# Performance work log

Measured on AMD Instinct MI355X. Metric: run time of the kernel, lower is better.

## Reference

```python
import jax, jax.numpy as jnp
import numpy as np
import math

B, L, D = 2, 4096, 1024
H, DK, DV = 4, 256, 256
CS = 32          # delta-rule chunk size
CONV = 4         # short conv kernel
FIR_S, FIR_L = 3, 31
GIN = D + 3 * DV # 1792 gate input dim
GH = D * 2 // 2  # 1024 gate hidden dim
MIN_LOCAL = 0.05


def dwconv(x, w):
    """Causal depthwise conv. x: [b,l,C], w: [C,k] -> [b,l,C]."""
    k = w.shape[-1]
    xf = jnp.pad(jnp.swapaxes(x, 1, 2), ((0, 0), (0, 0), (k - 1, 0)))
    y = jax.lax.conv_general_dilated(xf, w[:, None, :], (1,), 'VALID',
                                     dimension_numbers=('NCH', 'OIH', 'NCH'),
                                     feature_group_count=w.shape[0])
    return jnp.swapaxes(y, 1, 2)


def l2n(x):
    return x * jax.lax.rsqrt(jnp.sum(x * x, -1, keepdims=True) + 1e-12)


def delta_rule(q, k, v, beta):
    """Chunkwise O(N) delta rule. q,k: [b,h,L,dk], v: [b,h,L,dv], beta: [b,h,L]."""
    b, h, Lq, dk = q.shape
    dv = v.shape[-1]
    n = Lq // CS
    q, k = l2n(q), l2n(k)
    v = v * beta[..., None]
    kb = k * beta[..., None]
    rs = lambda t: t.reshape(b, h, n, CS, t.shape[-1])
    q, k, v, kb = rs(q), rs(k), rs(v), rs(kb)
    # block-local inverse of unit-lower-triangular (I + strict_lower(kb k^T))
    strict_lo = jnp.tril(jnp.ones((CS, CS), bool), -1)
    A = jnp.where(strict_lo, kb @ jnp.swapaxes(k, -1, -2), 0.0)
    eye = jnp.eye(CS, dtype=q.dtype)
    Tinv = jax.scipy.linalg.solve_triangular(
        eye + A, jnp.broadcast_to(eye, A.shape), lower=True, unit_diagonal=True)
    u = Tinv @ v
    w = Tinv @ kb
    strict_up = jnp.triu(jnp.ones((CS, CS), bool), 1)

    def step(S, xs):
        q_i, k_i, u_i, w_i = xs
        attn = jnp.where(strict_up, 0.0, q_i @ jnp.swapaxes(k_i, -1, -2))
        u_i = u_i - w_i @ S
        o_i = q_i @ S + attn @ u_i
        S = S + jnp.swapaxes(k_i, -1, -2) @ u_i
        return S, o_i

    mv = lambda t: jnp.moveaxis(t, 2, 0)  # scan over chunks
    S0 = jnp.zeros((b, h, dk, dv), q.dtype)
    _, out = jax.lax.scan(step, S0, (mv(q), mv(k), mv(u), mv(w)))
    return jnp.moveaxis(out, 0, 2).reshape(b, h, Lq, dv)


def _forward(hidden_states, q_proj_w, k_proj_w, v_proj_w, b_proj_w,
             q_conv_w, k_conv_w, v_conv_w, fir_short_w, fir_long_w,
             fg_w1, fg_b1, fg_w2, fg_b2, logit_temp, o_norm_w, o_proj_w):
    b, l, _ = hidden_states.shape
    hs = hidden_states
    q = jax.nn.silu(dwconv(hs @ q_proj_w.T, q_conv_w)).reshape(b, l, H, DK)
    k = jax.nn.silu(dwconv(hs @ k_proj_w.T, k_conv_w)).reshape(b, l, H, DK)
    v = jax.nn.silu(dwconv(hs @ v_proj_w.T, v_conv_w)).reshape(b, l, H, DV)
    beta = jax.nn.sigmoid(hs @ b_proj_w.T)  # [b,l,h]
    tr = lambda t: jnp.swapaxes(t, 1, 2)
    delta = tr(delta_rule(tr(q), tr(k), tr(v), jnp.swapaxes(beta, 1, 2)))
    fir = lambda x, w: dwconv(x.reshape(b, l, H * DV),
                              w.reshape(H * DV, -1)).reshape(b, l, H, DV)
    short = fir(v, fir_short_w)
    long_ = fir(v, fir_long_w)
    gate_in = jnp.concatenate([hs, short.mean(2), long_.mean(2), delta.mean(2)], -1)
    logits = jax.nn.gelu(gate_in @ fg_w1.T + fg_b1, approximate=False) @ fg_w2.T + fg_b2
    temp = jax.nn.softplus(logit_temp) + 1e-4
    wgt = jax.nn.softmax(logits / temp, -1)[:, :, None, :]  # [b,l,1,4]
    wgt = jnp.broadcast_to(wgt, (b, l, H, 4))
    # floor on local-path weights proportional to direct-value weight, renormalize
    floor = MIN_LOCAL * wgt[..., 3:4]
    wloc = jnp.maximum(wgt[..., :2], floor)
    wgt = jnp.concatenate([wloc, wgt[..., 2:]], -1)
    wgt = wgt / wgt.sum(-1, keepdims=True)
    o = (wgt[..., 0:1] * short + wgt[..., 1:2] * long_ +
         wgt[..., 2:3] * delta + wgt[..., 3:4] * v)
    # RMSNorm over head_v_dim
    o = o * jax.lax.rsqrt(jnp.mean(o * o, -1, keepdims=True) + 1e-5) * o_norm_w
    return o.reshape(b, l, H * DV) @ o_proj_w.T


def setup_inputs() -> dict:
    key = jax.random.key(0)
    ks = jax.random.split(key, 12)
    s = 0.02
    return {
        'hidden_states': jax.random.normal(ks[0], (B, L, D), jnp.float32),
        'q_proj_w': jax.random.normal(ks[1], (H * DK, D), jnp.float32) * s,
        'k_proj_w': jax.random.normal(ks[2], (H * DK, D), jnp.float32) * s,
        'v_proj_w': jax.random.normal(ks[3], (H * DV, D), jnp.float32) * s,
        'b_proj_w': jax.random.normal(ks[4], (H, D), jnp.float32) * s,
        'q_conv_w': jax.random.normal(ks[5], (H * DK, CONV), jnp.float32) * s,
        'k_conv_w': jax.random.normal(ks[6], (H * DK, CONV), jnp.float32) * s,
        'v_conv_w': jax.random.normal(ks[7], (H * DV, CONV), jnp.float32) * s,
        'fir_short_w': jnp.zeros((H, DV, FIR_S), jnp.float32).at[..., -1].set(1.0),
        'fir_long_w': jnp.zeros((H, DV, FIR_L), jnp.float32).at[..., -1].set(1.0),
        'fg_w1': jax.random.normal(ks[8], (GH, GIN), jnp.float32) * s,
        'fg_b1': jnp.zeros((GH,), jnp.float32),
        'fg_w2': jax.random.normal(ks[9], (4, GH), jnp.float32) * s,
        'fg_b2': jnp.array([-0.2, -0.2, 1.0, 3.0], jnp.float32),
        'logit_temp': jnp.full((1,), math.log(math.expm1(0.7)), jnp.float32),
        'o_norm_w': jnp.ones((DV,), jnp.float32),
        'o_proj_w': jax.random.normal(ks[10], (D, H * DV), jnp.float32) * s,
    }


def reference(hidden_states, q_proj_w, k_proj_w, v_proj_w, b_proj_w,
              q_conv_w, k_conv_w, v_conv_w, fir_short_w, fir_long_w,
              fg_w1, fg_b1, fg_w2, fg_b2, logit_temp, o_norm_w, o_proj_w):
    return _forward(hidden_states, q_proj_w, k_proj_w, v_proj_w, b_proj_w,
                    q_conv_w, k_conv_w, v_conv_w, fir_short_w, fir_long_w,
                    fg_w1, fg_b1, fg_w2, fg_b2, logit_temp, o_norm_w, o_proj_w)
```

## Files before the change

### kernel.cpp

```cpp
#include <hip/hip_runtime.h>
#include <cstdint>
#include <cstddef>

namespace {
constexpr int LB   = 4096;
constexpr int CS   = 32;
constexpr int NCH  = 128;
constexpr int GINC = 1792;
constexpr int GHC  = 1024;
}

__device__ __forceinline__ float dot4(float4 a, float4 b) {
  return a.x*b.x + a.y*b.y + a.z*b.z + a.w*b.w;
}

__global__ __launch_bounds__(256)
void gemm_bt(const float* __restrict__ A, const float* __restrict__ W,
             float* __restrict__ C, int M, int N, int K) {
  __shared__ float As[16][128];
  __shared__ float Bs[16][128];
  const int tid = threadIdx.x;
  const int bn = blockIdx.x * 128;
  const int bm = blockIdx.y * 128;
  const int tx = tid & 15, ty = tid >> 4;
  const int lr = tid >> 1, lk = (tid & 1) * 8;

  float acc[8][8];
  #pragma unroll
  for (int i = 0; i < 8; ++i)
    #pragma unroll
    for (int j = 0; j < 8; ++j) acc[i][j] = 0.f;

  const float* Ap = A + (size_t)(bm + lr) * K + lk;
  const float* Wp = W + (size_t)(bn + lr) * K + lk;

  for (int k0 = 0; k0 < K; k0 += 16) {
    float4 a0 = *(const float4*)(Ap + k0);
    float4 a1 = *(const float4*)(Ap + k0 + 4);
    float4 b0 = *(const float4*)(Wp + k0);
    float4 b1 = *(const float4*)(Wp + k0 + 4);
    __syncthreads();
    As[lk+0][lr]=a0.x; As[lk+1][lr]=a0.y; As[lk+2][lr]=a0.z; As[lk+3][lr]=a0.w;
    As[lk+4][lr]=a1.x; As[lk+5][lr]=a1.y; As[lk+6][lr]=a1.z; As[lk+7][lr]=a1.w;
    Bs[lk+0][lr]=b0.x; Bs[lk+1][lr]=b0.y; Bs[lk+2][lr]=b0.z; Bs[lk+3][lr]=b0.w;
    Bs[lk+4][lr]=b1.x; Bs[lk+5][lr]=b1.y; Bs[lk+6][lr]=b1.z; Bs[lk+7][lr]=b1.w;
    __syncthreads();
    #pragma unroll
    for (int kk = 0; kk < 16; ++kk) {
      float av[8], bv[8];
      *(float4*)(av)   = *(const float4*)&As[kk][ty*8];
      *(float4*)(av+4) = *(const float4*)&As[kk][ty*8+4];
      *(float4*)(bv)   = *(const float4*)&Bs[kk][tx*8];
      *(float4*)(bv+4) = *(const float4*)&Bs[kk][tx*8+4];
      #pragma unroll
      for (int i = 0; i < 8; ++i)
        #pragma unroll
        for (int j = 0; j < 8; ++j) acc[i][j] += av[i]*bv[j];
    }
  }

  #pragma unroll
  for (int i = 0; i < 8; ++i) {
    float* cp = C + (size_t)(bm + ty*8 + i) * N + bn + tx*8;
    *(float4*)cp     = make_float4(acc[i][0],acc[i][1],acc[i][2],acc[i][3]);
    *(float4*)(cp+4) = make_float4(acc[i][4],acc[i][5],acc[i][6],acc[i][7]);
  }
}

__global__ __launch_bounds__(256)
void gemm_gate(const float* __restrict__ hs, const float* __restrict__ sh,
               const float* __restrict__ lo, const float* __restrict__ de,
               const float* __restrict__ W, const float* __restrict__ bias,
               float* __restrict__ C) {
  const int M = LB, N = GHC, K = GINC;
  __shared__ float As[16][128];
  __shared__ float Bs[16][128];
  const int tid = threadIdx.x;
  const int bn = blockIdx.x * 128;
  const int bm = blockIdx.y * 128;
  const int tx = tid & 15, ty = tid >> 4;
  const int lr = tid >> 1, lk = (tid & 1) * 8;

  float acc[8][8];
  #pragma unroll
  for (int i = 0; i < 8; ++i)
    #pragma unroll
    for (int j = 0; j < 8; ++j) acc[i][j] = 0.f;

  const size_t arow = (size_t)(bm + lr) * 1024;
  const float* Wp = W + (size_t)(bn + lr) * K + lk;

  for (int k0 = 0; k0 < K; k0 += 16) {
    const int col = k0 + lk;
    float4 a0, a1;
    if (col < 1024) {
      const float* p = hs + arow + col;
      a0 = *(const float4*)p; a1 = *(const float4*)(p + 4);
    } else {
      const int sec = (col - 1024) >> 8;
      const int d   = (col - 1024) & 255;
      const float* p = (sec == 0 ? sh : (sec == 1 ? lo : de)) + arow + d;
      float4 q0 = *(const float4*)(p);       float4 q1 = *(const float4*)(p+4);
      float4 r0 = *(const float4*)(p+256);   float4 r1 = *(const float4*)(p+260);
      float4 s0 = *(const float4*)(p+512);   float4 s1 = *(const float4*)(p+516);
      float4 t0 = *(const float4*)(p+768);   float4 t1 = *(const float4*)(p+772);
      a0 = make_float4(0.25f*(q0.x+r0.x+s0.x+t0.x), 0.25f*(q0.y+r0.y+s0.y+t0.y),
                       0.25f*(q0.z+r0.z+s0.z+t0.z), 0.25f*(q0.w+r0.w+s0.w+t0.w));
      a1 = make_float4(0.25f*(q1.x+r1.x+s1.x+t1.x), 0.25f*(q1.y+r1.y+s1.y+t1.y),
                       0.25f*(q1.z+r1.z+s1.z+t1.z), 0.25f*(q1.w+r1.w+s1.w+t1.w));
    }
    float4 b0 = *(const float4*)(Wp + k0);
    float4 b1 = *(const float4*)(Wp + k0 + 4);
    __syncthreads();
    As[lk+0][lr]=a0.x; As[lk+1][lr]=a0.y; As[lk+2][lr]=a0.z; As[lk+3][lr]=a0.w;
    As[lk+4][lr]=a1.x; As[lk+5][lr]=a1.y; As[lk+6][lr]=a1.z; As[lk+7][lr]=a1.w;
    Bs[lk+0][lr]=b0.x; Bs[lk+1][lr]=b0.y; Bs[lk+2][lr]=b0.z; Bs[lk+3][lr]=b0.w;
    Bs[lk+4][lr]=b1.x; Bs[lk+5][lr]=b1.y; Bs[lk+6][lr]=b1.z; Bs[lk+7][lr]=b1.w;
    __syncthreads();
    #pragma unroll
    for (int kk = 0; kk < 16; ++kk) {
      float av[8], bv[8];
      *(float4*)(av)   = *(const float4*)&As[kk][ty*8];
      *(float4*)(av+4) = *(const float4*)&As[kk][ty*8+4];
      *(float4*)(bv)   = *(const float4*)&Bs[kk][tx*8];
      *(float4*)(bv+4) = *(const float4*)&Bs[kk][tx*8+4];
      #pragma unroll
      for (int i = 0; i < 8; ++i)
        #pragma unroll
        for (int j = 0; j < 8; ++j) acc[i][j] += av[i]*bv[j];
    }
  }

  float bvals[8];
  #pragma unroll
  for (int j = 0; j < 8; ++j) bvals[j] = bias[bn + tx*8 + j];
  #pragma unroll
  for (int i = 0; i < 8; ++i) {
    float* cp = C + (size_t)(bm + ty*8 + i) * N + bn + tx*8;
    float out[8];
    #pragma unroll
    for (int j = 0; j < 8; ++j) {
      float v = acc[i][j] + bvals[j];
      out[j] = 0.5f * v * (1.0f + erff(v * 0.70710678118654752f));
    }
    *(float4*)cp     = make_float4(out[0],out[1],out[2],out[3]);
    *(float4*)(cp+4) = make_float4(out[4],out[5],out[6],out[7]);
  }
}

__global__ __launch_bounds__(256)
void conv_silu_k(const float* __restrict__ x, const float* __restrict__ w,
                 float* __restrict__ y) {
  int idx = blockIdx.x * 256 + threadIdx.x;
  int c = idx & 1023;
  int l = idx >> 10;
  float w0 = w[c*4+0], w1 = w[c*4+1], w2 = w[c*4+2], w3 = w[c*4+3];
  float acc = x[(size_t)l*1024 + c] * w3;
  if (l >= 1) acc += x[(size_t)(l-1)*1024 + c] * w2;
  if (l >= 2) acc += x[(size_t)(l-2)*1024 + c] * w1;
  if (l >= 3) acc += x[(size_t)(l-3)*1024 + c] * w0;
  y[idx] = acc / (1.f + expf(-acc));
}

__global__ __launch_bounds__(256)
void beta_k(const float* __restrict__ hs, const float* __restrict__ bw,
            float* __restrict__ beta) {
  int row = blockIdx.x * 4 + (threadIdx.x >> 6);
  int ln  = threadIdx.x & 63;
  const float* xp = hs + (size_t)row * 1024 + ln*16;
  float a[4] = {0.f,0.f,0.f,0.f};
  #pragma unroll
  for (int t = 0; t < 4; ++t) {
    float4 xv = *(const float4*)(xp + t*4);
    #pragma unroll
    for (int h = 0; h < 4; ++h) {
      float4 wv = *(const float4*)(bw + (size_t)h*1024 + ln*16 + t*4);
      a[h] += dot4(xv, wv);
    }
  }
  #pragma unroll
  for (int h = 0; h < 4; ++h) {
    #pragma unroll
    for (int off = 32; off > 0; off >>= 1) a[h] += __shfl_xor(a[h], off, 64);
  }
  if (ln == 0) {
    #pragma unroll
    for (int h = 0; h < 4; ++h)
      beta[(size_t)row*4 + h] = 1.f / (1.f + expf(-a[h]));
  }
}

__global__ __launch_bounds__(256)
void delta_pre(float* __restrict__ q, float* __restrict__ k,
               const float* __restrict__ v, const float* __restrict__ beta,
               float* __restrict__ u, float* __restrict__ w,
               float* __restrict__ attn) {
  __shared__ float qs[32][260];
  __shared__ float ks[32][260];
  __shared__ float vs[32][260];
  __shared__ float Am[32][33];
  __shared__ float Ti[32][33];
  __shared__ float red[32][8];
  __shared__ float bet[32];

  const int bid = blockIdx.x;
  const int h  = bid & 3;
  const int c  = bid >> 2;
  const int tid = threadIdx.x;
  const int r  = tid >> 3;
  const int sg = tid & 7;

  const size_t base = (size_t)(c * CS) * 1024 + h * 256;
  float* qrow = q + base + (size_t)r * 1024 + sg * 32;
  float* krow = k + base + (size_t)r * 1024 + sg * 32;
  const float* vrow = v + base + (size_t)r * 1024 + sg * 32;

  #pragma unroll
  for (int t = 0; t < 8; ++t) {
    *(float4*)&qs[r][sg*32 + t*4] = *(const float4*)(qrow + t*4);
    *(float4*)&ks[r][sg*32 + t*4] = *(const float4*)(krow + t*4);
    *(float4*)&vs[r][sg*32 + t*4] = *(const float4*)(vrow + t*4);
  }
  if (tid < 32) bet[tid] = beta[(size_t)(c * CS + tid) * 4 + h];
  __syncthreads();

  {
    float p = 0.f;
    #pragma unroll
    for (int i = 0; i < 32; ++i) { float x = qs[r][sg*32+i]; p += x*x; }
    red[r][sg] = p;
  }
  __syncthreads();
  {
    float s = 1e-12f;
    #pragma unroll
    for (int i = 0; i < 8; ++i) s += red[r][i];
    float qn = rsqrtf(s);
    #pragma unroll
    for (int t = 0; t < 8; ++t) {
      float4 vq = *(float4*)&qs[r][sg*32 + t*4];
      vq.x*=qn; vq.y*=qn; vq.z*=qn; vq.w*=qn;
      *(float4*)&qs[r][sg*32 + t*4] = vq;
      *(float4*)(qrow + t*4) = vq;
    }
    float bb = bet[r];
    #pragma unroll
    for (int t = 0; t < 8; ++t) {
      float4 vv = *(float4*)&vs[r][sg*32 + t*4];
      vv.x*=bb; vv.y*=bb; vv.z*=bb; vv.w*=bb;
      *(float4*)&vs[r][sg*32 + t*4] = vv;
    }
  }
  __syncthreads();
  {
    float p = 0.f;
    #pragma unroll
    for (int i = 0; i < 32; ++i) { float x = ks[r][sg*32+i]; p += x*x; }
    red[r][sg] = p;
  }
  __syncthreads();
  {
    float s = 1e-12f;
    #pragma unroll
    for (int i = 0; i < 8; ++i) s += red[r][i];
    float kn = rsqrtf(s);
    #pragma unroll
    for (int t = 0; t < 8; ++t) {
      float4 vq = *(float4*)&ks[r][sg*32 + t*4];
      vq.x*=kn; vq.y*=kn; vq.z*=kn; vq.w*=kn;
      *(float4*)&ks[r][sg*32 + t*4] = vq;
      *(float4*)(krow + t*4) = vq;
    }
  }
  __syncthreads();

  {
    const int ti = tid >> 4, tj = tid & 15;
    const int r0 = ti*2, s0 = tj*2;
    float kk00=0,kk01=0,kk10=0,kk11=0,qk00=0,qk01=0,qk10=0,qk11=0;
    for (int d4 = 0; d4 < 64; ++d4) {
      float4 kr0 = *(const float4*)&ks[r0  ][d4*4];
      float4 kr1 = *(const float4*)&ks[r0+1][d4*4];
      float4 qr0 = *(const float4*)&qs[r0  ][d4*4];
      float4 qr1 = *(const float4*)&qs[r0+1][d4*4];
      float4 kc0 = *(const float4*)&ks[s0  ][d4*4];
      float4 kc1 = *(const float4*)&ks[s0+1][d4*4];
      kk00 += dot4(kr0,kc0); kk01 += dot4(kr0,kc1);
      kk10 += dot4(kr1,kc0); kk11 += dot4(kr1,kc1);
      qk00 += dot4(qr0,kc0); qk01 += dot4(qr0,kc1);
      qk10 += dot4(qr1,kc0); qk11 += dot4(qr1,kc1);
    }
    Am[r0  ][s0  ] = (r0   > s0  ) ? bet[r0  ]*kk00 : 0.f;
    Am[r0  ][s0+1] = (r0   > s0+1) ? bet[r0  ]*kk01 : 0.f;
    Am[r0+1][s0  ] = (r0+1 > s0  ) ? bet[r0+1]*kk10 : 0.f;
    Am[r0+1][s0+1] = (r0+1 > s0+1) ? bet[r0+1]*kk11 : 0.f;
    float* ap = attn + ((size_t)(h * NCH + c)) * 1024;
    ap[(r0  )*32 + s0  ] = (r0   >= s0  ) ? qk00 : 0.f;
    ap[(r0  )*32 + s0+1] = (r0   >= s0+1) ? qk01 : 0.f;
    ap[(r0+1)*32 + s0  ] = (r0+1 >= s0  ) ? qk10 : 0.f;
    ap[(r0+1)*32 + s0+1] = (r0+1 >= s0+1) ? qk11 : 0.f;
  }
  __syncthreads();

  if (tid < 32) {
    const int cc = tid;
    Ti[cc][cc] = 1.f;
    for (int rr = cc+1; rr < 32; ++rr) {
      float s = Am[rr][cc];
      for (int ss = cc+1; ss < rr; ++ss) s += Am[rr][ss] * Ti[ss][cc];
      Ti[rr][cc] = -s;
    }
  }
  __syncthreads();

  {
    float out[32];
    #pragma unroll
    for (int i = 0; i < 32; ++i) out[i] = vs[r][sg*32+i];
    for (int s2 = 0; s2 < r; ++s2) {
      float t = Ti[r][s2];
      #pragma unroll
      for (int t4 = 0; t4 < 8; ++t4) {
        float4 vv = *(const float4*)&vs[s2][sg*32 + t4*4];
        out[t4*4+0] += t*vv.x; out[t4*4+1] += t*vv.y;
        out[t4*4+2] += t*vv.z; out[t4*4+3] += t*vv.w;
      }
    }
    float* up = u + base + (size_t)r*1024 + sg*32;
    #pragma unroll
    for (int t4 = 0; t4 < 8; ++t4)
      *(float4*)(up + t4*4) = make_float4(out[t4*4],out[t4*4+1],out[t4*4+2],out[t4*4+3]);
  }
  {
    float out[32];
    float br = bet[r];
    #pragma unroll
    for (int i = 0; i < 32; ++i) out[i] = br * ks[r][sg*32+i];
    for (int s2 = 0; s2 < r; ++s2) {
      float t = Ti[r][s2] * bet[s2];
      #pragma unroll
      for (int t4 = 0; t4 < 8; ++t4) {
        float4 vv = *(const float4*)&ks[s2][sg*32 + t4*4];
        out[t4*4+0] += t*vv.x; out[t4*4+1] += t*vv.y;
        out[t4*4+2] += t*vv.z; out[t4*4+3] += t*vv.w;
      }
    }
    float* wp = w + base + (size_t)r*1024 + sg*32;
    #pragma unroll
    for (int t4 = 0; t4 < 8; ++t4)
      *(float4*)(wp + t4*4) = make_float4(out[t4*4],out[t4*4+1],out[t4*4+2],out[t4*4+3]);
  }
}

__device__ __forceinline__ void smul8(const float* __restrict__ row,
                                      const float* __restrict__ Sb,
                                      float acc[8]) {
  #pragma unroll
  for (int i4 = 0; i4 < 8; ++i4) {
    float4 wq = *(const float4*)(row + i4*4);
    float wv[4] = {wq.x, wq.y, wq.z, wq.w};
    #pragma unroll
    for (int t = 0; t < 4; ++t) {
      const float* sp = Sb + (i4*4 + t)*8;
      float4 s0 = *(const float4*)sp;
      float4 s1 = *(const float4*)(sp + 4);
      acc[0] += wv[t]*s0.x; acc[1] += wv[t]*s0.y;
      acc[2] += wv[t]*s0.z; acc[3] += wv[t]*s0.w;
      acc[4] += wv[t]*s1.x; acc[5] += wv[t]*s1.y;
      acc[6] += wv[t]*s1.z; acc[7] += wv[t]*s1.w;
    }
  }
}

__global__ __launch_bounds__(256)
void delta_scan(const float* __restrict__ q, const float* __restrict__ k,
                const float* __restrict__ w, const float* __restrict__ u,
                const float* __restrict__ attn, float* __restrict__ o) {
  __shared__ float ws_[32][260];
  __shared__ float qs[32][260];
  __shared__ float ks[32][260];
  __shared__ float Ssh[8*260];
  __shared__ float red[32][8][8];
  __shared__ float un[32][8];
  __shared__ float us[32][8];
  __shared__ float at[32][36];

  const int bid = blockIdx.x;
  const int h  = bid & 3;
  const int g  = bid >> 2;
  const int tid = threadIdx.x;
  const int r  = tid >> 3;
  const int sg = tid & 7;

  const size_t base = (size_t)h * 256;

  for (int i = tid; i < 8*260; i += 256) Ssh[i] = 0.f;

  for (int c = 0; c < NCH; ++c) {
    const size_t rowbase = base + (size_t)(c * CS) * 1024;
    const float* qp = q + rowbase + (size_t)r*1024 + sg*32;
    const float* kp = k + rowbase + (size_t)r*1024 + sg*32;
    const float* wp = w + rowbase + (size_t)r*1024 + sg*32;
    float4 qreg[8], kreg[8], wreg[8];
    #pragma unroll
    for (int t = 0; t < 8; ++t) {
      qreg[t] = *(const float4*)(qp + t*4);
      kreg[t] = *(const float4*)(kp + t*4);
      wreg[t] = *(const float4*)(wp + t*4);
    }
    float uval = u[rowbase + (size_t)r*1024 + g*8 + sg];
    float4 areg = *(const float4*)(attn + ((size_t)(h*NCH + c))*1024 + tid*4);

    __syncthreads();
    #pragma unroll
    for (int t = 0; t < 8; ++t) {
      *(float4*)&qs[r][sg*32 + t*4] = qreg[t];
      *(float4*)&ks[r][sg*32 + t*4] = kreg[t];
      *(float4*)&ws_[r][sg*32 + t*4] = wreg[t];
    }
    us[r][sg] = uval;
    at[r][sg*4+0] = areg.x; at[r][sg*4+1] = areg.y;
    at[r][sg*4+2] = areg.z; at[r][sg*4+3] = areg.w;
    __syncthreads();

    {
      float acc[8];
      #pragma unroll
      for (int j = 0; j < 8; ++j) acc[j] = 0.f;
      smul8(&ws_[r][sg*32], &Ssh[sg*260], acc);
      *(float4*)&red[r][sg][0] = make_float4(acc[0],acc[1],acc[2],acc[3]);
      *(float4*)&red[r][sg][4] = make_float4(acc[4],acc[5],acc[6],acc[7]);
    }
    __syncthreads();
    {
      float t = 0.f;
      #pragma unroll
      for (int o2 = 0; o2 < 8; ++o2) t += red[r][o2][sg];
      un[r][sg] = us[r][sg] - t;
    }
    __syncthreads();
    {
      float acc[8];
      #pragma unroll
      for (int j = 0; j < 8; ++j) acc[j] = 0.f;
      smul8(&qs[r][sg*32], &Ssh[sg*260], acc);
      #pragma unroll
      for (int t2 = 0; t2 < 4; ++t2) {
        int s2 = sg*4 + t2;
        float a = at[r][s2];
        float4 u0 = *(const float4*)&un[s2][0];
        float4 u1 = *(const float4*)&un[s2][4];
        acc[0] += a*u0.x; acc[1] += a*u0.y; acc[2] += a*u0.z; acc[3] += a*u0.w;
        acc[4] += a*u1.x; acc[5] += a*u1.y; acc[6] += a*u1.z; acc[7] += a*u1.w;
      }
      *(float4*)&red[r][sg][0] = make_float4(acc[0],acc[1],acc[2],acc[3]);
      *(float4*)&red[r][sg][4] = make_float4(acc[4],acc[5],acc[6],acc[7]);
    }
    __syncthreads();
    {
      float t = 0.f;
      #pragma unroll
      for (int o2 = 0; o2 < 8; ++o2) t += red[r][o2][sg];
      o[rowbase + (size_t)r*1024 + g*8 + sg] = t;
    }
    {
      const int dk = tid;
      float a2[8];
      #pragma unroll
      for (int j = 0; j < 8; ++j) a2[j] = 0.f;
      #pragma unroll 4
      for (int r2 = 0; r2 < 32; ++r2) {
        float kv = ks[r2][dk];
        float4 u0 = *(const float4*)&un[r2][0];
        float4 u1 = *(const float4*)&un[r2][4];
        a2[0] += kv*u0.x; a2[1] += kv*u0.y; a2[2] += kv*u0.z; a2[3] += kv*u0.w;
        a2[4] += kv*u1.x; a2[5] += kv*u1.y; a2[6] += kv*u1.z; a2[7] += kv*u1.w;
      }
      float* sp = &Ssh[(dk>>5)*260 + (dk&31)*8];
      float4 s0 = *(float4*)sp, s1 = *(float4*)(sp+4);
      s0.x += a2[0]; s0.y += a2[1]; s0.z += a2[2]; s0.w += a2[3];
      s1.x += a2[4]; s1.y += a2[5]; s1.z += a2[6]; s1.w += a2[7];
      *(float4*)sp = s0; *(float4*)(sp+4) = s1;
    }
  }
}

template<int KF>
__global__ __launch_bounds__(256)
void fir_k(const float* __restrict__ x, const float* __restrict__ wf,
           float* __restrict__ y) {
  int idx = blockIdx.x * 256 + threadIdx.x;
  int c = idx & 1023;
  int l = idx >> 10;
  const float* wp = wf + (size_t)c * KF;
  float acc = 0.f;
  #pragma unroll
  for (int j = 0; j < KF; ++j) {
    int ls = l - (KF-1) + j;
    if (ls >= 0) acc += x[(size_t)ls*1024 + c] * wp[j];
  }
  y[idx] = acc;
}

__global__ __launch_bounds__(256)
void logit_k(const float* __restrict__ hid, const float* __restrict__ w2,
             const float* __restrict__ b2, const float* __restrict__ lt,
             float* __restrict__ wgt) {
  int row = blockIdx.x * 4 + (threadIdx.x >> 6);
  int ln  = threadIdx.x & 63;
  const float* hp = hid + (size_t)row * 1024 + ln*16;
  float a[4] = {0.f,0.f,0.f,0.f};
  #pragma unroll
  for (int t = 0; t < 4; ++t) {
    float4 hv = *(const float4*)(hp + t*4);
    #pragma unroll
    for (int cc = 0; cc < 4; ++cc) {
      float4 wv = *(const float4*)(w2 + (size_t)cc*1024 + ln*16 + t*4);
      a[cc] += dot4(hv, wv);
    }
  }
  #pragma unroll
  for (int cc = 0; cc < 4; ++cc) {
    #pragma unroll
    for (int off = 32; off > 0; off >>= 1) a[cc] += __shfl_xor(a[cc], off, 64);
  }
  if (ln == 0) {
    float x = lt[0];
    float temp = (x > 20.f ? x : log1pf(expf(x))) + 1e-4f;
    float lg[4];
    #pragma unroll
    for (int cc = 0; cc < 4; ++cc) lg[cc] = (a[cc] + b2[cc]) / temp;
    float m = fmaxf(fmaxf(lg[0],lg[1]), fmaxf(lg[2],lg[3]));
    float e0 = expf(lg[0]-m), e1 = expf(lg[1]-m), e2 = expf(lg[2]-m), e3 = expf(lg[3]-m);
    float inv = 1.f / (e0+e1+e2+e3);
    float s0 = e0*inv, s1 = e1*inv, s2 = e2*inv, s3 = e3*inv;
    float fl = 0.05f * s3;
    float w0 = fmaxf(s0, fl), w1 = fmaxf(s1, fl);
    float tot = 1.f / (w0 + w1 + s2 + s3);
    float* wp = wgt + (size_t)row*4;
    wp[0] = w0*tot; wp[1] = w1*tot; wp[2] = s2*tot; wp[3] = s3*tot;
  }
}

__global__ __launch_bounds__(256)
void mix_k(const float* __restrict__ sh, const float* __restrict__ lo,
           const float* __restrict__ de, const float* __restrict__ v,
           const float* __restrict__ wgt, const float* __restrict__ onw,
           float* __restrict__ o) {
  int bid = blockIdx.x;
  int l = bid >> 2, h = bid & 3;
  int d = threadIdx.x;
  size_t off = (size_t)l*1024 + h*256 + d;
  const float* wp = wgt + (size_t)l*4;
  float w0 = wp[0], w1 = wp[1], w2 = wp[2], w3 = wp[3];
  float val = w0*sh[off] + w1*lo[off] + w2*de[off] + w3*v[off];
  __shared__ float rd[4];
  float ss = val*val;
  #pragma unroll
  for (int m = 32; m > 0; m >>= 1) ss += __shfl_xor(ss, m, 64);
  if ((threadIdx.x & 63) == 0) rd[threadIdx.x >> 6] = ss;
  __syncthreads();
  float tot = rd[0] + rd[1] + rd[2] + rd[3];
  float sc = rsqrtf(tot * (1.f/256.f) + 1e-5f);
  o[off] = val * sc * onw[d];
}

extern "C" void kernel_launch(void* const* d_in, const int* in_sizes, int n_in,
                              void* d_out, int out_size, void* d_ws, size_t ws_size,
                              hipStream_t stream) {
  (void)in_sizes; (void)n_in; (void)out_size; (void)ws_size;
  const float* hs   = (const float*)d_in[0];
  const float* qw   = (const float*)d_in[1];
  const float* kw   = (const float*)d_in[2];
  const float* vw   = (const float*)d_in[3];
  const float* bw   = (const float*)d_in[4];
  const float* qcw  = (const float*)d_in[5];
  const float* kcw  = (const float*)d_in[6];
  const float* vcw  = (const float*)d_in[7];
  const float* fsw  = (const float*)d_in[8];
  const float* flw  = (const float*)d_in[9];
  const float* fgw1 = (const float*)d_in[10];
  const float* fgb1 = (const float*)d_in[11];
  const float* fgw2 = (const float*)d_in[12];
  const float* fgb2 = (const float*)d_in[13];
  const float* ltmp = (const float*)d_in[14];
  const float* onw  = (const float*)d_in[15];
  const float* ow   = (const float*)d_in[16];

  float* ws0 = (float*)d_ws;
  const size_t SZB = (size_t)LB * 1024;
  float* A    = ws0;
  float* qb   = ws0 + SZB;
  float* kb2  = ws0 + 2*SZB;
  float* vb   = ws0 + 3*SZB;
  float* ub   = ws0 + 4*SZB;
  float* wb   = ws0 + 5*SZB;
  float* att  = ws0 + 6*SZB;
  float* betab= att + (size_t)4*NCH*1024;
  float* wgtb = betab + (size_t)LB*4;

  dim3 blk(256);
  dim3 gg(1024/128, LB/128);
  const int ELT = LB*1024/256;

  for (int b = 0; b < 2; ++b) {
    const float* hsb = hs + (size_t)b * LB * 1024;
    float* outb = (float*)d_out + (size_t)b * LB * 1024;

    gemm_bt<<<gg, blk, 0, stream>>>(hsb, qw, A, LB, 1024, 1024);
    conv_silu_k<<<dim3(ELT), blk, 0, stream>>>(A, qcw, qb);
    gemm_bt<<<gg, blk, 0, stream>>>(hsb, kw, A, LB, 1024, 1024);
    conv_silu_k<<<dim3(ELT), blk, 0, stream>>>(A, kcw, kb2);
    gemm_bt<<<gg, blk, 0, stream>>>(hsb, vw, A, LB, 1024, 1024);
    conv_silu_k<<<dim3(ELT), blk, 0, stream>>>(A, vcw, vb);

    beta_k<<<dim3(LB/4), blk, 0, stream>>>(hsb, bw, betab);
    delta_pre<<<dim3(512), blk, 0, stream>>>(qb, kb2, vb, betab, ub, wb, att);
    delta_scan<<<dim3(128), blk, 0, stream>>>(qb, kb2, wb, ub, att, A);

    fir_k<3><<<dim3(ELT), blk, 0, stream>>>(vb, fsw, qb);
    fir_k<31><<<dim3(ELT), blk, 0, stream>>>(vb, flw, kb2);

    gemm_gate<<<gg, blk, 0, stream>>>(hsb, qb, kb2, A, fgw1, fgb1, ub);
    logit_k<<<dim3(LB/4), blk, 0, stream>>>(ub, fgw2, fgb2, ltmp, wgtb);
    mix_k<<<dim3(LB*4), blk, 0, stream>>>(qb, kb2, A, vb, wgtb, onw, wb);

    gemm_bt<<<gg, blk, 0, stream>>>(wb, ow, outb, LB, 1024, 1024);
  }
}
```

Baseline: 5.468 ms.

## Batch delta-rule kernels across both sequences and shorten the scan critical path

When the workspace is large enough, q/k/v/u/w buffers for both batch elements are kept so delta_pre and delta_scan run once over the batch with twice as many blocks. This fills more of the GPU during the serial scan. delta_pre now precomputes q - attn·w per chunk, so each scan step needs one fused pass over the state and one reduction instead of two dependent rounds with extra barriers. It also rotates the shared-memory access order to reduce bank conflicts. The cost is a larger workspace requirement and a fallback path that keeps the old per-batch schedule.

```diff
diff --git a/kernel.cpp b/kernel.cpp
--- a/kernel.cpp
+++ b/kernel.cpp
@@ -8,6 +8,7 @@
 constexpr int NCH  = 128;
 constexpr int GINC = 1792;
 constexpr int GHC  = 1024;
+constexpr size_t SZB = (size_t)LB * 1024;
 }
 
 __device__ __forceinline__ float dot4(float4 a, float4 b) {
@@ -72,7 +73,7 @@
                const float* __restrict__ lo, const float* __restrict__ de,
                const float* __restrict__ W, const float* __restrict__ bias,
                float* __restrict__ C) {
-  const int M = LB, N = GHC, K = GINC;
+  const int N = GHC, K = GINC;
   __shared__ float As[16][128];
   __shared__ float Bs[16][128];
   const int tid = threadIdx.x;
@@ -200,28 +201,31 @@
   __shared__ float vs[32][260];
   __shared__ float Am[32][33];
   __shared__ float Ti[32][33];
+  __shared__ float ats[32][33];
   __shared__ float red[32][8];
   __shared__ float bet[32];
 
   const int bid = blockIdx.x;
+  const int b  = bid >> 9;
   const int h  = bid & 3;
-  const int c  = bid >> 2;
+  const int c  = (bid >> 2) & 127;
   const int tid = threadIdx.x;
   const int r  = tid >> 3;
   const int sg = tid & 7;
 
-  const size_t base = (size_t)(c * CS) * 1024 + h * 256;
+  const size_t base = (size_t)b * SZB + (size_t)(c * CS) * 1024 + h * 256;
   float* qrow = q + base + (size_t)r * 1024 + sg * 32;
   float* krow = k + base + (size_t)r * 1024 + sg * 32;
   const float* vrow = v + base + (size_t)r * 1024 + sg * 32;
 
   #pragma unroll
   for (int t = 0; t < 8; ++t) {
-    *(float4*)&qs[r][sg*32 + t*4] = *(const float4*)(qrow + t*4);
-    *(float4*)&ks[r][sg*32 + t*4] = *(const float4*)(krow + t*4);
-    *(float4*)&vs[r][sg*32 + t*4] = *(const float4*)(vrow + t*4);
-  }
-  if (tid < 32) bet[tid] = beta[(size_t)(c * CS + tid) * 4 + h];
+    int tr = (t + sg) & 7;
+    *(float4*)&qs[r][sg*32 + tr*4] = *(const float4*)(qrow + tr*4);
+    *(float4*)&ks[r][sg*32 + tr*4] = *(const float4*)(krow + tr*4);
+    *(float4*)&vs[r][sg*32 + tr*4] = *(const float4*)(vrow + tr*4);
+  }
+  if (tid < 32) bet[tid] = beta[((size_t)b*LB + c*CS + tid)*4 + h];
   __syncthreads();
 
   {
@@ -238,17 +242,18 @@
     float qn = rsqrtf(s);
     #pragma unroll
     for (int t = 0; t < 8; ++t) {
-      float4 vq = *(float4*)&qs[r][sg*32 + t*4];
+      int tr = (t + sg) & 7;
+      float4 vq = *(float4*)&qs[r][sg*32 + tr*4];
       vq.x*=qn; vq.y*=qn; vq.z*=qn; vq.w*=qn;
-      *(float4*)&qs[r][sg*32 + t*4] = vq;
-      *(float4*)(qrow + t*4) = vq;
+      *(float4*)&qs[r][sg*32 + tr*4] = vq;
     }
     float bb = bet[r];
     #pragma unroll
     for (int t = 0; t < 8; ++t) {
-      float4 vv = *(float4*)&vs[r][sg*32 + t*4];
+      int tr = (t + sg) & 7;
+      float4 vv = *(float4*)&vs[r][sg*32 + tr*4];
       vv.x*=bb; vv.y*=bb; vv.z*=bb; vv.w*=bb;
-      *(float4*)&vs[r][sg*32 + t*4] = vv;
+      *(float4*)&vs[r][sg*32 + tr*4] = vv;
     }
   }
   __syncthreads();
@@ -266,10 +271,11 @@
     float kn = rsqrtf(s);
     #pragma unroll
     for (int t = 0; t < 8; ++t) {
-      float4 vq = *(float4*)&ks[r][sg*32 + t*4];
+      int tr = (t + sg) & 7;
+      float4 vq = *(float4*)&ks[r][sg*32 + tr*4];
       vq.x*=kn; vq.y*=kn; vq.z*=kn; vq.w*=kn;
-      *(float4*)&ks[r][sg*32 + t*4] = vq;
-      *(float4*)(krow + t*4) = vq;
+      *(float4*)&ks[r][sg*32 + tr*4] = vq;
+      *(float4*)(krow + tr*4) = vq;
     }
   }
   __syncthreads();
@@ -294,11 +300,17 @@
     Am[r0  ][s0+1] = (r0   > s0+1) ? bet[r0  ]*kk01 : 0.f;
     Am[r0+1][s0  ] = (r0+1 > s0  ) ? bet[r0+1]*kk10 : 0.f;
     Am[r0+1][s0+1] = (r0+1 > s0+1) ? bet[r0+1]*kk11 : 0.f;
-    float* ap = attn + ((size_t)(h * NCH + c)) * 1024;
-    ap[(r0  )*32 + s0  ] = (r0   >= s0  ) ? qk00 : 0.f;
-    ap[(r0  )*32 + s0+1] = (r0   >= s0+1) ? qk01 : 0.f;
-    ap[(r0+1)*32 + s0  ] = (r0+1 >= s0  ) ? qk10 : 0.f;
-    ap[(r0+1)*32 + s0+1] = (r0+1 >= s0+1) ? qk11 : 0.f;
+    float a00 = (r0   >= s0  ) ? qk00 : 0.f;
+    float a01 = (r0   >= s0+1) ? qk01 : 0.f;
+    float a10 = (r0+1 >= s0  ) ? qk10 : 0.f;
+    float a11 = (r0+1 >= s0+1) ? qk11 : 0.f;
+    ats[r0  ][s0  ] = a00;  ats[r0  ][s0+1] = a01;
+    ats[r0+1][s0  ] = a10;  ats[r0+1][s0+1] = a11;
+    float* ap = attn + (((size_t)b*4 + h) * NCH + c) * 1024;
+    ap[(r0  )*32 + s0  ] = a00;
+    ap[(r0  )*32 + s0+1] = a01;
+    ap[(r0+1)*32 + s0  ] = a10;
+    ap[(r0+1)*32 + s0+1] = a11;
   }
   __syncthreads();
 
@@ -316,14 +328,18 @@
   {
     float out[32];
     #pragma unroll
-    for (int i = 0; i < 32; ++i) out[i] = vs[r][sg*32+i];
+    for (int t = 0; t < 8; ++t) {
+      int tr = (t + sg) & 7;
+      *(float4*)&out[tr*4] = *(const float4*)&vs[r][sg*32 + tr*4];
+    }
     for (int s2 = 0; s2 < r; ++s2) {
       float t = Ti[r][s2];
       #pragma unroll
       for (int t4 = 0; t4 < 8; ++t4) {
-        float4 vv = *(const float4*)&vs[s2][sg*32 + t4*4];
-        out[t4*4+0] += t*vv.x; out[t4*4+1] += t*vv.y;
-        out[t4*4+2] += t*vv.z; out[t4*4+3] += t*vv.w;
+        int tr = (t4 + sg) & 7;
+        float4 vv = *(const float4*)&vs[s2][sg*32 + tr*4];
+        out[tr*4+0] += t*vv.x; out[tr*4+1] += t*vv.y;
+        out[tr*4+2] += t*vv.z; out[tr*4+3] += t*vv.w;
       }
     }
     float* up = u + base + (size_t)r*1024 + sg*32;
@@ -331,6 +347,8 @@
     for (int t4 = 0; t4 < 8; ++t4)
       *(float4*)(up + t4*4) = make_float4(out[t4*4],out[t4*4+1],out[t4*4+2],out[t4*4+3]);
   }
+  __syncthreads();
+
   {
     float out[32];
     float br = bet[r];
@@ -340,35 +358,41 @@
       float t = Ti[r][s2] * bet[s2];
       #pragma unroll
       for (int t4 = 0; t4 < 8; ++t4) {
-        float4 vv = *(const float4*)&ks[s2][sg*32 + t4*4];
-        out[t4*4+0] += t*vv.x; out[t4*4+1] += t*vv.y;
-        out[t4*4+2] += t*vv.z; out[t4*4+3] += t*vv.w;
+        int tr = (t4 + sg) & 7;
+        float4 vv = *(const float4*)&ks[s2][sg*32 + tr*4];
+        out[tr*4+0] += t*vv.x; out[tr*4+1] += t*vv.y;
+        out[tr*4+2] += t*vv.z; out[tr*4+3] += t*vv.w;
       }
     }
     float* wp = w + base + (size_t)r*1024 + sg*32;
     #pragma unroll
+    for (int t4 = 0; t4 < 8; ++t4) {
+      *(float4*)(wp + t4*4) = make_float4(out[t4*4],out[t4*4+1],out[t4*4+2],out[t4*4+3]);
+      *(float4*)&vs[r][sg*32 + t4*4] = *(const float4*)&out[t4*4];
+    }
+  }
+  __syncthreads();
+
+  {
+    float out[32];
+    #pragma unroll
+    for (int t = 0; t < 8; ++t) {
+      int tr = (t + sg) & 7;
+      *(float4*)&out[tr*4] = *(const float4*)&qs[r][sg*32 + tr*4];
+    }
+    for (int s2 = 0; s2 <= r; ++s2) {
+      float a = ats[r][s2];
+      #pragma unroll
+      for (int t4 = 0; t4 < 8; ++t4) {
+        int tr = (t4 + sg) & 7;
+        float4 vv = *(const float4*)&vs[s2][sg*32 + tr*4];
+        out[tr*4+0] -= a*vv.x; out[tr*4+1] -= a*vv.y;
+        out[tr*4+2] -= a*vv.z; out[tr*4+3] -= a*vv.w;
+      }
+    }
+    #pragma unroll
     for (int t4 = 0; t4 < 8; ++t4)
-      *(float4*)(wp + t4*4) = make_float4(out[t4*4],out[t4*4+1],out[t4*4+2],out[t4*4+3]);
-  }
-}
-
-__device__ __forceinline__ void smul8(const float* __restrict__ row,
-                                      const float* __restrict__ Sb,
-                                      float acc[8]) {
-  #pragma unroll
-  for (int i4 = 0; i4 < 8; ++i4) {
-    float4 wq = *(const float4*)(row + i4*4);
-    float wv[4] = {wq.x, wq.y, wq.z, wq.w};
-    #pragma unroll
-    for (int t = 0; t < 4; ++t) {
-      const float* sp = Sb + (i4*4 + t)*8;
-      float4 s0 = *(const float4*)sp;
-      float4 s1 = *(const float4*)(sp + 4);
-      acc[0] += wv[t]*s0.x; acc[1] += wv[t]*s0.y;
-      acc[2] += wv[t]*s0.z; acc[3] += wv[t]*s0.w;
-      acc[4] += wv[t]*s1.x; acc[5] += wv[t]*s1.y;
-      acc[6] += wv[t]*s1.z; acc[7] += wv[t]*s1.w;
-    }
+      *(float4*)(qrow + t4*4) = make_float4(out[t4*4],out[t4*4+1],out[t4*4+2],out[t4*4+3]);
   }
 }
 
@@ -380,19 +404,21 @@
   __shared__ float qs[32][260];
   __shared__ float ks[32][260];
   __shared__ float Ssh[8*260];
-  __shared__ float red[32][8][8];
+  __shared__ float red[2][32][68];
   __shared__ float un[32][8];
-  __shared__ float us[32][8];
+  __shared__ float us[32][12];
   __shared__ float at[32][36];
 
   const int bid = blockIdx.x;
+  const int b  = bid >> 7;
   const int h  = bid & 3;
-  const int g  = bid >> 2;
+  const int g  = (bid >> 2) & 31;
   const int tid = threadIdx.x;
   const int r  = tid >> 3;
   const int sg = tid & 7;
 
-  const size_t base = (size_t)h * 256;
+  const size_t base = (size_t)b * SZB + (size_t)h * 256;
+  const size_t aoff = ((size_t)b*4 + h) * NCH * 1024;
 
   for (int i = tid; i < 8*260; i += 256) Ssh[i] = 0.f;
 
@@ -409,14 +435,15 @@
       wreg[t] = *(const float4*)(wp + t*4);
     }
     float uval = u[rowbase + (size_t)r*1024 + g*8 + sg];
-    float4 areg = *(const float4*)(attn + ((size_t)(h*NCH + c))*1024 + tid*4);
+    float4 areg = *(const float4*)(attn + aoff + (size_t)c*1024 + tid*4);
 
     __syncthreads();
     #pragma unroll
     for (int t = 0; t < 8; ++t) {
-      *(float4*)&qs[r][sg*32 + t*4] = qreg[t];
-      *(float4*)&ks[r][sg*32 + t*4] = kreg[t];
-      *(float4*)&ws_[r][sg*32 + t*4] = wreg[t];
+      int tr = (t + sg) & 7;
+      *(float4*)&qs[r][sg*32 + tr*4]  = qreg[tr];
+      *(float4*)&ks[r][sg*32 + tr*4]  = kreg[tr];
+      *(float4*)&ws_[r][sg*32 + tr*4] = wreg[tr];
     }
     us[r][sg] = uval;
     at[r][sg*4+0] = areg.x; at[r][sg*4+1] = areg.y;
@@ -424,45 +451,59 @@
     __syncthreads();
 
     {
-      float acc[8];
-      #pragma unroll
-      for (int j = 0; j < 8; ++j) acc[j] = 0.f;
-      smul8(&ws_[r][sg*32], &Ssh[sg*260], acc);
-      *(float4*)&red[r][sg][0] = make_float4(acc[0],acc[1],acc[2],acc[3]);
-      *(float4*)&red[r][sg][4] = make_float4(acc[4],acc[5],acc[6],acc[7]);
+      float accw[8], accq[8];
+      #pragma unroll
+      for (int j = 0; j < 8; ++j) { accw[j] = 0.f; accq[j] = 0.f; }
+      #pragma unroll
+      for (int t2 = 0; t2 < 4; ++t2) {
+        int s2 = sg*4 + ((t2 + r) & 3);
+        float a = at[r][s2];
+        float4 u0 = *(const float4*)&us[s2][0];
+        float4 u1 = *(const float4*)&us[s2][4];
+        accq[0] += a*u0.x; accq[1] += a*u0.y; accq[2] += a*u0.z; accq[3] += a*u0.w;
+        accq[4] += a*u1.x; accq[5] += a*u1.y; accq[6] += a*u1.z; accq[7] += a*u1.w;
+      }
+      #pragma unroll
+      for (int i4 = 0; i4 < 8; ++i4) {
+        int ir = (i4 + sg) & 7;
+        float4 wq = *(const float4*)&ws_[r][sg*32 + ir*4];
+        float4 qq = *(const float4*)&qs[r][sg*32 + ir*4];
+        float wv[4] = {wq.x,wq.y,wq.z,wq.w};
+        float qv[4] = {qq.x,qq.y,qq.z,qq.w};
+        #pragma unroll
+        for (int t = 0; t < 4; ++t) {
+          const float* sp = &Ssh[sg*260 + (ir*4 + t)*8];
+          float4 s0 = *(const float4*)sp;
+          float4 s1 = *(const float4*)(sp + 4);
+          accw[0] += wv[t]*s0.x; accw[1] += wv[t]*s0.y;
+          accw[2] += wv[t]*s0.z; accw[3] += wv[t]*s0.w;
+          accw[4] += wv[t]*s1.x; accw[5] += wv[t]*s1.y;
+          accw[6] += wv[t]*s1.z; accw[7] += wv[t]*s1.w;
+          accq[0] += qv[t]*s0.x; accq[1] += qv[t]*s0.y;
+          accq[2] += qv[t]*s0.z; accq[3] += qv[t]*s0.w;
+          accq[4] += qv[t]*s1.x; accq[5] += qv[t]*s1.y;
+          accq[6] += qv[t]*s1.z; accq[7] += qv[t]*s1.w;
+        }
+      }
+      *(float4*)&red[0][r][sg*8]     = make_float4(accw[0],accw[1],accw[2],accw[3]);
+      *(float4*)&red[0][r][sg*8+4]   = make_float4(accw[4],accw[5],accw[6],accw[7]);
+      *(float4*)&red[1][r][sg*8]     = make_float4(accq[0],accq[1],accq[2],accq[3]);
+      *(float4*)&red[1][r][sg*8+4]   = make_float4(accq[4],accq[5],accq[6],accq[7]);
     }
     __syncthreads();
+
     {
-      float t = 0.f;
-      #pragma unroll
-      for (int o2 = 0; o2 < 8; ++o2) t += red[r][o2][sg];
-      un[r][sg] = us[r][sg] - t;
+      float tw = 0.f, tq = 0.f;
+      #pragma unroll
+      for (int o2 = 0; o2 < 8; ++o2) {
+        tw += red[0][r][o2*8 + sg];
+        tq += red[1][r][o2*8 + sg];
+      }
+      un[r][sg] = us[r][sg] - tw;
+      o[rowbase + (size_t)r*1024 + g*8 + sg] = tq;
     }
     __syncthreads();
-    {
-      float acc[8];
-      #pragma unroll
-      for (int j = 0; j < 8; ++j) acc[j] = 0.f;
-      smul8(&qs[r][sg*32], &Ssh[sg*260], acc);
-      #pragma unroll
-      for (int t2 = 0; t2 < 4; ++t2) {
-        int s2 = sg*4 + t2;
-        float a = at[r][s2];
-        float4 u0 = *(const float4*)&un[s2][0];
-        float4 u1 = *(const float4*)&un[s2][4];
-        acc[0] += a*u0.x; acc[1] += a*u0.y; acc[2] += a*u0.z; acc[3] += a*u0.w;
-        acc[4] += a*u1.x; acc[5] += a*u1.y; acc[6] += a*u1.z; acc[7] += a*u1.w;
-      }
-      *(float4*)&red[r][sg][0] = make_float4(acc[0],acc[1],acc[2],acc[3]);
-      *(float4*)&red[r][sg][4] = make_float4(acc[4],acc[5],acc[6],acc[7]);
-    }
-    __syncthreads();
-    {
-      float t = 0.f;
-      #pragma unroll
-      for (int o2 = 0; o2 < 8; ++o2) t += red[r][o2][sg];
-      o[rowbase + (size_t)r*1024 + g*8 + sg] = t;
-    }
+
     {
       const int dk = tid;
       float a2[8];
@@ -568,7 +609,7 @@
 extern "C" void kernel_launch(void* const* d_in, const int* in_sizes, int n_in,
                               void* d_out, int out_size, void* d_ws, size_t ws_size,
                               hipStream_t stream) {
-  (void)in_sizes; (void)n_in; (void)out_size; (void)ws_size;
+  (void)in_sizes; (void)n_in; (void)out_size;
   const float* hs   = (const float*)d_in[0];
   const float* qw   = (const float*)d_in[1];
   const float* kw   = (const float*)d_in[2];
@@ -588,43 +629,84 @@
   const float* ow   = (const float*)d_in[16];
 
   float* ws0 = (float*)d_ws;
-  const size_t SZB = (size_t)LB * 1024;
-  float* A    = ws0;
-  float* qb   = ws0 + SZB;
-  float* kb2  = ws0 + 2*SZB;
-  float* vb   = ws0 + 3*SZB;
-  float* ub   = ws0 + 4*SZB;
-  float* wb   = ws0 + 5*SZB;
-  float* att  = ws0 + 6*SZB;
-  float* betab= att + (size_t)4*NCH*1024;
-  float* wgtb = betab + (size_t)LB*4;
-
   dim3 blk(256);
   dim3 gg(1024/128, LB/128);
   const int ELT = LB*1024/256;
 
-  for (int b = 0; b < 2; ++b) {
-    const float* hsb = hs + (size_t)b * LB * 1024;
-    float* outb = (float*)d_out + (size_t)b * LB * 1024;
-
-    gemm_bt<<<gg, blk, 0, stream>>>(hsb, qw, A, LB, 1024, 1024);
-    conv_silu_k<<<dim3(ELT), blk, 0, stream>>>(A, qcw, qb);
-    gemm_bt<<<gg, blk, 0, stream>>>(hsb, kw, A, LB, 1024, 1024);
-    conv_silu_k<<<dim3(ELT), blk, 0, stream>>>(A, kcw, kb2);
-    gemm_bt<<<gg, blk, 0, stream>>>(hsb, vw, A, LB, 1024, 1024);
-    conv_silu_k<<<dim3(ELT), blk, 0, stream>>>(A, vcw, vb);
-
-    beta_k<<<dim3(LB/4), blk, 0, stream>>>(hsb, bw, betab);
-    delta_pre<<<dim3(512), blk, 0, stream>>>(qb, kb2, vb, betab, ub, wb, att);
-    delta_scan<<<dim3(128), blk, 0, stream>>>(qb, kb2, wb, ub, att, A);
-
-    fir_k<3><<<dim3(ELT), blk, 0, stream>>>(vb, fsw, qb);
-    fir_k<31><<<dim3(ELT), blk, 0, stream>>>(vb, flw, kb2);
-
-    gemm_gate<<<gg, blk, 0, stream>>>(hsb, qb, kb2, A, fgw1, fgb1, ub);
-    logit_k<<<dim3(LB/4), blk, 0, stream>>>(ub, fgw2, fgb2, ltmp, wgtb);
-    mix_k<<<dim3(LB*4), blk, 0, stream>>>(qb, kb2, A, vb, wgtb, onw, wb);
-
-    gemm_bt<<<gg, blk, 0, stream>>>(wb, ow, outb, LB, 1024, 1024);
-  }
-}
+  const size_t ATT = (size_t)4*NCH*1024;
+  const size_t need = (1 + 10) * SZB + 2*ATT + 2*(size_t)LB*4 + (size_t)LB*4;
+  const bool merged = ws_size >= need * 4;
+
+  if (merged) {
+    float* A    = ws0;
+    float* qb   = ws0 + SZB;
+    float* kb2  = ws0 + 3*SZB;
+    float* vb   = ws0 + 5*SZB;
+    float* ub   = ws0 + 7*SZB;
+    float* wb   = ws0 + 9*SZB;
+    float* att  = ws0 + 11*SZB;
+    float* betab= att + 2*ATT;
+    float* wgtb = betab + 2*(size_t)LB*4;
+
+    for (int b = 0; b < 2; ++b) {
+      const float* hsb = hs + (size_t)b * SZB;
+      gemm_bt<<<gg, blk, 0, stream>>>(hsb, qw, A, LB, 1024, 1024);
+      conv_silu_k<<<dim3(ELT), blk, 0, stream>>>(A, qcw, qb + b*SZB);
+      gemm_bt<<<gg, blk, 0, stream>>>(hsb, kw, A, LB, 1024, 1024);
+      conv_silu_k<<<dim3(ELT), blk, 0, stream>>>(A, kcw, kb2 + b*SZB);
+      gemm_bt<<<gg, blk, 0, stream>>>(hsb, vw, A, LB, 1024, 1024);
+      conv_silu_k<<<dim3(ELT), blk, 0, stream>>>(A, vcw, vb + b*SZB);
+      beta_k<<<dim3(LB/4), blk, 0, stream>>>(hsb, bw, betab + b*(size_t)LB*4);
+    }
+    delta_pre<<<dim3(1024), blk, 0, stream>>>(qb, kb2, vb, betab, ub, wb, att);
+    delta_scan<<<dim3(256), blk, 0, stream>>>(qb, kb2, wb, ub, att, ub);
+
+    for (int b = 0; b < 2; ++b) {
+      const float* hsb = hs + (size_t)b * SZB;
+      float* q_ = qb + b*SZB; float* k_ = kb2 + b*SZB;
+      float* v_ = vb + b*SZB; float* u_ = ub + b*SZB; float* w_ = wb + b*SZB;
+      float* outb = (float*)d_out + (size_t)b * SZB;
+      fir_k<3><<<dim3(ELT), blk, 0, stream>>>(v_, fsw, q_);
+      fir_k<31><<<dim3(ELT), blk, 0, stream>>>(v_, flw, k_);
+      gemm_gate<<<gg, blk, 0, stream>>>(hsb, q_, k_, u_, fgw1, fgb1, A);
+      logit_k<<<dim3(LB/4), blk, 0, stream>>>(A, fgw2, fgb2, ltmp, wgtb);
+      mix_k<<<dim3(LB*4), blk, 0, stream>>>(q_, k_, u_, v_, wgtb, onw, w_);
+      gemm_bt<<<gg, blk, 0, stream>>>(w_, ow, outb, LB, 1024, 1024);
+    }
+  } else {
+    float* A    = ws0;
+    float* qb   = ws0 + SZB;
+    float* kb2  = ws0 + 2*SZB;
+    float* vb   = ws0 + 3*SZB;
+    float* ub   = ws0 + 4*SZB;
+    float* wb   = ws0 + 5*SZB;
+    float* att  = ws0 + 6*SZB;
+    float* betab= att + ATT;
+    float* wgtb = betab + (size_t)LB*4;
+
+    for (int b = 0; b < 2; ++b) {
+      const float* hsb = hs + (size_t)b * SZB;
+      float* outb = (float*)d_out + (size_t)b * SZB;
+
+      gemm_bt<<<gg, blk, 0, stream>>>(hsb, qw, A, LB, 1024, 1024);
+      conv_silu_k<<<dim3(ELT), blk, 0, stream>>>(A, qcw, qb);
+      gemm_bt<<<gg, blk, 0, stream>>>(hsb, kw, A, LB, 1024, 1024);
+      conv_silu_k<<<dim3(ELT), blk, 0, stream>>>(A, kcw, kb2);
+      gemm_bt<<<gg, blk, 0, stream>>>(hsb, vw, A, LB, 1024, 1024);
+      conv_silu_k<<<dim3(ELT), blk, 0, stream>>>(A, vcw, vb);
+
+      beta_k<<<dim3(LB/4), blk, 0, stream>>>(hsb, bw, betab);
+      delta_pre<<<dim3(512), blk, 0, stream>>>(qb, kb2, vb, betab, ub, wb, att);
+      delta_scan<<<dim3(128), blk, 0, stream>>>(qb, kb2, wb, ub, att, ub);
+
+      fir_k<3><<<dim3(ELT), blk, 0, stream>>>(vb, fsw, qb);
+      fir_k<31><<<dim3(ELT), blk, 0, stream>>>(vb, flw, kb2);
+
+      gemm_gate<<<gg, blk, 0, stream>>>(hsb, qb, kb2, ub, fgw1, fgb1, A);
+      logit_k<<<dim3(LB/4), blk, 0, stream>>>(A, fgw2, fgb2, ltmp, wgtb);
+      mix_k<<<dim3(LB*4), blk, 0, stream>>>(qb, kb2, ub, vb, wgtb, onw, wb);
+
+      gemm_bt<<<gg, blk, 0, stream>>>(wb, ow, outb, LB, 1024, 1024);
+    }
+  }
+}
```

New measurement: 5.691 ms. +4.1%, slower.
